# Optimization experiments

Measured on AMD Instinct MI355X. Metric: run time of the kernel, lower is better.

The kernel has to match this reference:

```python
import jax, jax.numpy as jnp
import numpy as np

B, C, H, W = 8, 128, 64, 64
NWIN, HEADS, QKDIM, KVPW, TOPK = 8, 8, 128, 4, 16
SCALE = QKDIM ** -0.5

def _ln(x, g, b, eps):
    mu = x.mean(-1, keepdims=True)
    var = ((x - mu) ** 2).mean(-1, keepdims=True)
    return (x - mu) * jax.lax.rsqrt(var + eps) * g + b

def _conv(x, w, b, pad, groups=1):
    y = jax.lax.conv_general_dilated(x, w, (1, 1), [(pad, pad), (pad, pad)],
        dimension_numbers=('NCHW', 'OIHW', 'NCHW'), feature_group_count=groups)
    return y + b[None, :, None, None]

def setup_inputs():
    key = jax.random.key(0)
    ks = jax.random.split(key, 8)
    s = 0.05
    return {
        't1': jax.random.normal(ks[0], (B, C, H, W), jnp.float32),
        't2': jax.random.normal(ks[1], (B, C, H, W), jnp.float32),
        'pos_w': jax.random.normal(ks[2], (C, 1, 3, 3), jnp.float32) * s,
        'pos_b': jnp.zeros((C,), jnp.float32),
        'cat_w': jax.random.normal(ks[3], (C, 2 * C, 3, 3), jnp.float32) * s,
        'cat_b': jnp.zeros((C,), jnp.float32),
        'ln_cat_g': jnp.ones((C,), jnp.float32),
        'ln_cat_b': jnp.zeros((C,), jnp.float32),
        'ln1_g': jnp.ones((C,), jnp.float32),
        'ln1_b': jnp.zeros((C,), jnp.float32),
        'qkv_w': jax.random.normal(ks[4], (2 * QKDIM + C, C), jnp.float32) * s,
        'qkv_b': jnp.zeros((2 * QKDIM + C,), jnp.float32),
        'lepe_w': jax.random.normal(ks[5], (C, 1, 5, 5), jnp.float32) * s,
        'lepe_b': jnp.zeros((C,), jnp.float32),
        'wo_w': jax.random.normal(ks[6], (C, C), jnp.float32) * s,
        'wo_b': jnp.zeros((C,), jnp.float32),
    }

def _bra_cross(q_in, kv_in, qkv_w, qkv_b, lepe_w, lepe_b, wo_w, wo_b):
    # Bi-level routing cross attention: queries from q_in, keys/values from kv_in (NHWC).
    p = NWIN; wh, ww = H // p, W // p; p2 = p * p
    q = (q_in @ qkv_w.T + qkv_b)[..., :QKDIM]          # (B,H,W,QKDIM)
    kv = (kv_in @ qkv_w.T + qkv_b)[..., QKDIM:]        # (B,H,W,QKDIM+C)

    def win(x):
        c = x.shape[-1]
        return x.reshape(B, p, wh, p, ww, c).transpose(0, 1, 3, 2, 4, 5).reshape(B, p2, wh, ww, c)

    qw, kvw = win(q), win(kv)
    q_pix = qw.reshape(B, p2, wh * ww, QKDIM)
    # adaptive avg-pool each window's kv to KVPW x KVPW ('ada_avgpool')
    f = wh // KVPW
    kv_pix = kvw.reshape(B, p2, KVPW, f, KVPW, f, QKDIM + C).mean(axis=(3, 5))
    kv_pix = kv_pix.reshape(B, p2, KVPW * KVPW, QKDIM + C)
    q_win = qw.mean(axis=(2, 3))                        # (B,p2,QKDIM)
    k_win = kvw[..., :QKDIM].mean(axis=(2, 3))
    # LePE: depthwise 5x5 conv on full-resolution v
    v_full = kv[..., QKDIM:].transpose(0, 3, 1, 2)
    lepe = _conv(v_full, lepe_w, lepe_b, 2, groups=C).transpose(0, 2, 3, 1)
    # region-level routing (detached: diff_routing=False)
    logits = jnp.einsum('bpc,bqc->bpq',
                        jax.lax.stop_gradient(q_win) * SCALE,
                        jax.lax.stop_gradient(k_win))
    _, r_idx = jax.lax.top_k(logits, TOPK)              # (B,p2,TOPK)
    # gather kv of routed regions: (B,p2,TOPK,KVPW^2,QKDIM+C)
    kv_sel = jax.vmap(lambda kvp, idx: kvp[idx])(kv_pix, r_idx)
    k_sel = kv_sel[..., :QKDIM].reshape(B, p2, TOPK * KVPW * KVPW, HEADS, QKDIM // HEADS)
    v_sel = kv_sel[..., QKDIM:].reshape(B, p2, TOPK * KVPW * KVPW, HEADS, C // HEADS)
    q_h = q_pix.reshape(B, p2, wh * ww, HEADS, QKDIM // HEADS)
    attn = jnp.einsum('bpqmc,bpkmc->bpmqk', q_h * SCALE, k_sel)
    attn = jax.nn.softmax(attn, axis=-1)
    out = jnp.einsum('bpmqk,bpkmc->bpqmc', attn, v_sel).reshape(B, p2, wh, ww, C)
    out = out.reshape(B, p, p, wh, ww, C).transpose(0, 1, 3, 2, 4, 5).reshape(B, H, W, C)
    out = out + lepe
    return out @ wo_w.T + wo_b

def reference(t1, t2, pos_w, pos_b, cat_w, cat_b, ln_cat_g, ln_cat_b,
              ln1_g, ln1_b, qkv_w, qkv_b, lepe_w, lepe_b, wo_w, wo_b):
    # Block.forward: depthwise conv positional embedding
    t1 = t1 + _conv(t1, pos_w, pos_b, 1, groups=C)
    t2 = t2 + _conv(t2, pos_w, pos_b, 1, groups=C)
    t1n = t1.transpose(0, 2, 3, 1)
    t2n = t2.transpose(0, 2, 3, 1)
    # RGBConcatConv: cat on channel-last, 3x3 conv, relu(LayerNorm)
    xc = jnp.concatenate([t1n, t2n], axis=3).transpose(0, 3, 1, 2)
    xc = _conv(xc, cat_w, cat_b, 1).transpose(0, 2, 3, 1)
    x = jax.nn.relu(_ln(xc, ln_cat_g, ln_cat_b, 1e-5))
    attn = _bra_cross(_ln(t1n, ln1_g, ln1_b, 1e-6), _ln(t2n, ln1_g, ln1_b, 1e-6),
                      qkv_w, qkv_b, lepe_w, lepe_b, wo_w, wo_b)
    x = x + attn
    return x.transpose(0, 3, 1, 2)
```

## Files before the change

### kernel.cpp

```cpp
#include <hip/hip_runtime.h>
#include <math.h>

typedef unsigned short ushort_t;
typedef __attribute__((ext_vector_type(4))) float f32x4;
typedef __attribute__((ext_vector_type(16))) float f32x16;
typedef __attribute__((ext_vector_type(8))) short bf16x8;

constexpr int B = 8, C = 128, H = 64, W = 64;
constexpr int HEADS = 8, TOPK = 16;
constexpr int P2 = 64;
constexpr float SCALE = 0.0883883476483184405f;

constexpr size_t NPIX    = (size_t)B * H * W;
constexpr size_t OFF_T1C = 0;
constexpr size_t OFF_T2C = OFF_T1C + NPIX * 128;
constexpr size_t OFF_X   = OFF_T2C + NPIX * 128;
constexpr size_t OFF_QB  = OFF_X   + NPIX * 128;
constexpr size_t OFF_KV  = OFF_QB  + NPIX * 64;
constexpr size_t OFF_KVP = OFF_KV  + NPIX * 256;
constexpr size_t OFF_RW1 = OFF_KVP + 524288;
constexpr size_t OFF_RW2 = OFF_RW1 + 524288;
constexpr size_t OFF_KVPT= OFF_KVP + (size_t)B * P2 * 16 * 256;
constexpr size_t OFF_QW  = OFF_KVPT+ (size_t)B * P2 * 128 * 16 / 2;
constexpr size_t OFF_KW  = OFF_QW  + (size_t)B * P2 * 128;
constexpr size_t OFF_RIDX= OFF_KW  + (size_t)B * P2 * 128;
constexpr size_t OFF_WCB = OFF_RIDX+ (size_t)B * P2 * TOPK;
constexpr size_t OFF_QKVB= OFF_WCB + (size_t)9 * 256 * 128;
constexpr size_t OFF_WOB = OFF_QKVB+ (size_t)384 * 128 / 2;
constexpr size_t OFF_T1B = OFF_WOB + 8192;
constexpr size_t OFF_T2B = OFF_T1B + NPIX * 64;

__device__ inline ushort_t f2bf(float f) {
    unsigned u = __float_as_uint(f);
    unsigned r = u + 0x7FFFu + ((u >> 16) & 1u);
    return (ushort_t)(r >> 16);
}
__device__ inline float bf2f(ushort_t u) {
    return __uint_as_float((unsigned)u << 16);
}

__global__ void transpose_weights(const float* __restrict__ qkv_w,
                                  const float* __restrict__ wo_w,
                                  const float* __restrict__ cat_w,
                                  ushort_t* __restrict__ qkvB,
                                  ushort_t* __restrict__ woB,
                                  ushort_t* __restrict__ wcat2) {
    int idx = blockIdx.x * 256 + threadIdx.x;
    if (idx < 384 * 128) qkvB[idx] = f2bf(qkv_w[idx]);
    if (idx < 128 * 128) woB[idx]  = f2bf(wo_w[idx]);
    if (idx < 36 * 8 * 128 * 8) {
        int i  = idx & 7;
        int n  = (idx >> 3) & 127;
        int r  = idx >> 10;
        int lg = r & 3;
        int kk = (r >> 2) & 1;
        int sdd = r >> 3;
        int dd = sdd % 9, q = sdd / 9;
        int ci = q * 64 + kk * 32 + lg * 8 + i;
        wcat2[idx] = f2bf(cat_w[((size_t)n * 256 + ci) * 9 + dd]);
    }
}

__global__ __launch_bounds__(256) void pos_conv_k(
        const float* __restrict__ t1, const float* __restrict__ t2,
        const float* __restrict__ w, const float* __restrict__ bias,
        float* __restrict__ out1, float* __restrict__ out2,
        ushort_t* __restrict__ ob1, ushort_t* __restrict__ ob2) {
    __shared__ float tile[4][32][33];
    int z = blockIdx.z;
    int which = z >> 7, rem = z & 127;
    int b = rem >> 4, y0 = (rem & 15) * 4;
    const float* in = which ? t2 : t1;
    float* outNHWC = which ? out2 : out1;
    ushort_t* outB = which ? ob2 : ob1;
    int c0 = blockIdx.y * 32, x0 = blockIdx.x * 32;
    int tx = threadIdx.x & 31, tg = threadIdx.x >> 5;
    int x = x0 + tx;
    for (int i = 0; i < 4; i++) {
        int cl = tg * 4 + i, c = c0 + cl;
        const float* base = in + (size_t)(b * C + c) * H * W;
        float wv[9];
#pragma unroll
        for (int j = 0; j < 9; j++) wv[j] = w[c * 9 + j];
        float rows[6][3];
#pragma unroll
        for (int yy = 0; yy < 6; yy++) {
            int gy = y0 - 1 + yy;
            bool yok = (gy >= 0 && gy < H);
#pragma unroll
            for (int dx = 0; dx < 3; dx++) {
                int gx = x + dx - 1;
                rows[yy][dx] = (yok && gx >= 0 && gx < W) ? base[gy * W + gx] : 0.f;
            }
        }
        float bb = bias[c];
#pragma unroll
        for (int k = 0; k < 4; k++) {
            float acc = rows[k + 1][1] + bb;
#pragma unroll
            for (int dy = 0; dy < 3; dy++)
#pragma unroll
                for (int dx = 0; dx < 3; dx++)
                    acc += rows[k + dy][dx] * wv[dy * 3 + dx];
            tile[k][cl][tx] = acc;
        }
    }
    __syncthreads();
    for (int k = 0; k < 4; k++)
        for (int i = 0; i < 4; i++) {
            int xl = tg * 4 + i;
            float val = tile[k][tx][xl];
            size_t idx = ((size_t)(b * H + y0 + k) * W + x0 + xl) * 128 + c0 + tx;
            outNHWC[idx] = val;
            outB[idx] = f2bf(val);
        }
}

__global__ __launch_bounds__(512) void catconv_mfma_k(
        const ushort_t* __restrict__ t1b, const ushort_t* __restrict__ t2b,
        const ushort_t* __restrict__ wcat2,
        const float* __restrict__ cat_b,
        const float* __restrict__ g, const float* __restrict__ beta,
        ushort_t* __restrict__ xbuf) {
    __shared__ __align__(16) unsigned char smem[64 * 132 * 4 + 2 * 64 * 4];
    int t = threadIdx.x;
    int lane = t & 63, wv = t >> 6;
    int mw = wv >> 2, nw = wv & 3;
    int l15 = lane & 15, lg = lane >> 4;
    int b = blockIdx.z, y0 = blockIdx.y * 8, x0 = blockIdx.x * 8;

    f32x4 acc[2][2];
#pragma unroll
    for (int m = 0; m < 2; m++)
#pragma unroll
        for (int cf = 0; cf < 2; cf++)
            acc[m][cf] = (f32x4){0.f, 0.f, 0.f, 0.f};

    int pyA[2], pxA[2];
#pragma unroll
    for (int m = 0; m < 2; m++) {
        int p = mw * 32 + m * 16 + l15;
        pyA[m] = p >> 3; pxA[m] = p & 7;
    }

    for (int q = 0; q < 4; q++) {
        __syncthreads();
        {
            const ushort_t* src = (q < 2 ? t1b : t2b);
            int coff = (q & 1) * 64;
            for (int e = t; e < 800; e += 512) {
                int pix = e >> 3, c8 = e & 7;
                int hy = pix / 10, hx = pix - hy * 10;
                int gy = y0 - 1 + hy, gx = x0 - 1 + hx;
                uint4 v = make_uint4(0u, 0u, 0u, 0u);
                if (gy >= 0 && gy < H && gx >= 0 && gx < W)
                    v = *reinterpret_cast<const uint4*>(
                        src + ((size_t)(b * H + gy) * W + gx) * 128 + coff + c8 * 8);
                *reinterpret_cast<uint4*>(smem + pix * 144 + c8 * 16) = v;
            }
        }
        __syncthreads();
#pragma unroll
// ... 1 lines not shown
            int dy = dd / 3, dx = dd - dy * 3;
            const ushort_t* wb = wcat2 + ((size_t)((q * 9 + dd) * 8 + lg) * 128) * 8;
            bf16x8 bfr[2][2];
#pragma unroll
            for (int kk = 0; kk < 2; kk++)
#pragma unroll
                for (int cf = 0; cf < 2; cf++)
                    bfr[kk][cf] = *reinterpret_cast<const bf16x8*>(
                        wb + (size_t)kk * 4096 + (nw * 32 + cf * 16 + l15) * 8);
            bf16x8 af[2][2];
#pragma unroll
            for (int m = 0; m < 2; m++)
#pragma unroll
                for (int kk = 0; kk < 2; kk++)
                    af[m][kk] = *reinterpret_cast<const bf16x8*>(
                        smem + ((pyA[m] + dy) * 10 + pxA[m] + dx) * 144 + kk * 64 + lg * 16);
#pragma unroll
            for (int m = 0; m < 2; m++)
#pragma unroll
                for (int cf = 0; cf < 2; cf++)
#pragma unroll
                    for (int kk = 0; kk < 2; kk++)
                        acc[m][cf] = __builtin_amdgcn_mfma_f32_16x16x32_bf16(
                            af[m][kk], bfr[kk][cf], acc[m][cf], 0, 0, 0);
        }
    }

    __syncthreads();
    float* res = (float*)smem;
    float* mstat = (float*)(smem + 64 * 132 * 4);
#pragma unroll
    for (int cf = 0; cf < 2; cf++) {
        int n = nw * 32 + cf * 16 + l15;
        float cb = cat_b[n];
#pragma unroll
        for (int m = 0; m < 2; m++)
#pragma unroll
            for (int i = 0; i < 4; i++)
                res[(mw * 32 + m * 16 + lg * 4 + i) * 132 + n] = acc[m][cf][i] + cb;
    }
    __syncthreads();
    {
        int pix = t >> 3, sub = t & 7;
        float s1 = 0.f;
#pragma unroll
        for (int j = 0; j < 16; j++) s1 += res[pix * 132 + sub + j * 8];
        s1 += __shfl_xor(s1, 1, 64);
        s1 += __shfl_xor(s1, 2, 64);
        s1 += __shfl_xor(s1, 4, 64);
        float mean = s1 * (1.f / 128.f);
        float s2 = 0.f;
#pragma unroll
        for (int j = 0; j < 16; j++) {
            float d = res[pix * 132 + sub + j * 8] - mean;
            s2 += d * d;
        }
        s2 += __shfl_xor(s2, 1, 64);
        s2 += __shfl_xor(s2, 2, 64);
        s2 += __shfl_xor(s2, 4, 64);
        float inv = rsqrtf(s2 * (1.f / 128.f) + 1e-5f);
        if (sub == 0) { mstat[pix] = mean; mstat[64 + pix] = inv; }
    }
    __syncthreads();
    {
        int c = t & 127, pg = t >> 7;
        float gg = g[c], bb = beta[c];
        for (int j = 0; j < 16; j++) {
            int p2 = j * 4 + pg;
            float v = (res[p2 * 132 + c] - mstat[p2]) * mstat[64 + p2] * gg + bb;
            int py = p2 >> 3, px = p2 & 7;
            xbuf[((size_t)(b * H + y0 + py) * W + x0 + px) * 128 + c] = f2bf(fmaxf(v, 0.f));
        }
    }
}

__global__ __launch_bounds__(256) void ln_qkv_both_k(
        const float* __restrict__ t1c, const float* __restrict__ t2c,
        const float* __restrict__ g, const float* __restrict__ beta,
        const ushort_t* __restrict__ wB,
        const float* __restrict__ bias,
        ushort_t* __restrict__ outQ,
        ushort_t* __restrict__ outKV,
        float* __restrict__ rw1, float* __restrict__ rw2) {
    __shared__ __align__(16) unsigned char ash[64 * 272];
    int t = threadIdx.x;
    int lane = t & 63, wv = t >> 6;
    int which = blockIdx.y;
    const float* in = which ? t2c : t1c;
    float* rw = which ? rw2 : rw1;
    size_t p0 = (size_t)blockIdx.x * 64;
    int bb_ = blockIdx.x >> 6, yy_ = blockIdx.x & 63;
    {
        int row = t >> 2, sub = t & 3;
        const float* src = in + (p0 + row) * 128 + sub * 32;
        float4 v[8];
        float s = 0.f;
#pragma unroll
        for (int j = 0; j < 8; j++) {
            v[j] = *reinterpret_cast<const float4*>(src + j * 4);
            s += v[j].x + v[j].y + v[j].z + v[j].w;
        }
        s += __shfl_xor(s, 1, 64); s += __shfl_xor(s, 2, 64);
        float mean = s * (1.f / 128.f);
        float s2 = 0.f;
#pragma unroll
        for (int j = 0; j < 8; j++) {
            float dx = v[j].x - mean, dy = v[j].y - mean;
            float dz = v[j].z - mean, dw = v[j].w - mean;
            s2 += dx * dx + dy * dy + dz * dz + dw * dw;
        }
        s2 += __shfl_xor(s2, 1, 64); s2 += __shfl_xor(s2, 2, 64);
        float inv = rsqrtf(s2 * (1.f / 128.f) + 1e-6f);
        int wj = wv * 2 + (lane >> 5);
        bool writer = (lane & 28) == 0;
        float* rwp = rw + (((size_t)(bb_ * 8 + wj) * 64 + yy_) * 128) + sub * 32;
#pragma unroll
        for (int j = 0; j < 8; j++) {
            int c = sub * 32 + j * 4;
            float4 gv = *reinterpret_cast<const float4*>(g + c);
            float4 bv = *reinterpret_cast<const float4*>(beta + c);
            float o0 = (v[j].x - mean) * inv * gv.x + bv.x;
            float o1 = (v[j].y - mean) * inv * gv.y + bv.y;
            float o2 = (v[j].z - mean) * inv * gv.z + bv.z;
            float o3 = (v[j].w - mean) * inv * gv.w + bv.w;
            uint2 pk;
            pk.x = (unsigned)f2bf(o0) | ((unsigned)f2bf(o1) << 16);
            pk.y = (unsigned)f2bf(o2) | ((unsigned)f2bf(o3) << 16);
            *reinterpret_cast<uint2*>(ash + row * 272 + c * 2) = pk;
            float r0 = o0, r1 = o1, r2 = o2, r3 = o3;
#pragma unroll
            for (int m = 4; m <= 16; m <<= 1) {
                r0 += __shfl_xor(r0, m, 64);
                r1 += __shfl_xor(r1, m, 64);
                r2 += __shfl_xor(r2, m, 64);
                r3 += __shfl_xor(r3, m, 64);
            }
            if (writer)
                *reinterpret_cast<float4*>(rwp + j * 4) = make_float4(r0, r1, r2, r3);
        }
    }
    __syncthreads();
    int l15 = lane & 15, lg = lane >> 4;
    if (which == 0) {
        f32x4 acc[4][2];
#pragma unroll
        for (int mt = 0; mt < 4; mt++)
#pragma unroll
            for (int nn = 0; nn < 2; nn++)
                acc[mt][nn] = (f32x4){0.f, 0.f, 0.f, 0.f};
#pragma unroll
        for (int ks = 0; ks < 4; ks++) {
            bf16x8 af[4];
#pragma unroll
            for (int mt = 0; mt < 4; mt++)
                af[mt] = *reinterpret_cast<const bf16x8*>(
                    ash + (mt * 16 + l15) * 272 + ks * 64 + lg * 16);
#pragma unroll
            for (int nn = 0; nn < 2; nn++) {
                int n = (wv * 2 + nn) * 16 + l15;
                bf16x8 bfr = *reinterpret_cast<const bf16x8*>(
                    wB + (size_t)n * 128 + ks * 32 + lg * 8);
#pragma unroll
                for (int mt = 0; mt < 4; mt++)
                    acc[mt][nn] = __builtin_amdgcn_mfma_f32_16x16x32_bf16(
                        af[mt], bfr, acc[mt][nn], 0, 0, 0);
            }
        }
#pragma unroll
        for (int nn = 0; nn < 2; nn++) {
            int cg = (wv * 2 + nn) * 16 + l15;
            float bv = bias[cg];
#pragma unroll
            for (int mt = 0; mt < 4; mt++)
#pragma unroll
                for (int i = 0; i < 4; i++) {
                    size_t pix = p0 + mt * 16 + lg * 4 + i;
                    outQ[pix * 128 + cg] = f2bf((acc[mt][nn][i] + bv) * SCALE);
                }
        }
    } else {
        f32x4 acc[4][4];
#pragma unroll
        for (int mt = 0; mt < 4; mt++)
#pragma unroll
            for (int nn = 0; nn < 4; nn++)
                acc[mt][nn] = (f32x4){0.f, 0.f, 0.f, 0.f};
#pragma unroll
        for (int ks = 0; ks < 4; ks++) {
            bf16x8 af[4];
#pragma unroll
            for (int mt = 0; mt < 4; mt++)
                af[mt] = *reinterpret_cast<const bf16x8*>(
                    ash + (mt * 16 + l15) * 272 + ks * 64 + lg * 16);
#pragma unroll
            for (int nn = 0; nn < 4; nn++) {
                int n = 128 + (wv * 4 + nn) * 16 + l15;
                bf16x8 bfr = *reinterpret_cast<const bf16x8*>(
                    wB + (size_t)n * 128 + ks * 32 + lg * 8);
#pragma unroll
                for (int mt = 0; mt < 4; mt++)
                    acc[mt][nn] = __builtin_amdgcn_mfma_f32_16x16x32_bf16(
                        af[mt], bfr, acc[mt][nn], 0, 0, 0);
            }
        }
#pragma unroll
        for (int nn = 0; nn < 4; nn++) {
            int cg = (wv * 4 + nn) * 16 + l15;
            float bv = bias[128 + cg];
#pragma unroll
            for (int mt = 0; mt < 4; mt++)
#pragma unroll
                for (int i = 0; i < 4; i++) {
                    size_t pix = p0 + mt * 16 + lg * 4 + i;
                    outKV[pix * 256 + cg] = f2bf(acc[mt][nn][i] + bv);
                }
        }
    }
}

__global__ __launch_bounds__(256) void route_gemm_k(
        const float* __restrict__ rw1, const float* __restrict__ rw2,
        const float* __restrict__ qkv_w, const float* __restrict__ qkv_b,
        float* __restrict__ qwin, float* __restrict__ kwin) {
    __shared__ float msh[2][8][128];
    int b = blockIdx.y, wi = blockIdx.x;
    int t = threadIdx.x;
    for (int i = t; i < 8 * 128; i += 256) {
        int r = i >> 7, c = i & 127;
        size_t off = (((size_t)(b * 8 + r) * 64) + wi * 8) * 128 + c;
        float s1 = 0.f, s2 = 0.f;
#pragma unroll
        for (int rr = 0; rr < 8; rr++) {
            s1 += rw1[off + rr * 128];
            s2 += rw2[off + rr * 128];
        }
        msh[0][r][c] = s1 * (1.f / 64.f);
        msh[1][r][c] = s2 * (1.f / 64.f);
    }
    __syncthreads();
    int c = t;
    int which = c >> 7;
    const float* wrow = qkv_w + (size_t)c * 128;
    float acc[8];
#pragma unroll
    for (int r = 0; r < 8; r++) acc[r] = 0.f;
    for (int k = 0; k < 128; k++) {
        float wv_ = wrow[k];
#pragma unroll
        for (int r = 0; r < 8; r++) acc[r] += msh[which][r][k] * wv_;
    }
    float bv = qkv_b[c];
#pragma unroll
    for (int r = 0; r < 8; r++) {
        size_t o = ((size_t)b * 64 + wi * 8 + r) * 128 + (c & 127);
        (which ? kwin : qwin)[o] = acc[r] + bv;
    }
}

__global__ __launch_bounds__(64) void route_k(const float* __restrict__ q_win,
                                              const float* __restrict__ k_win,
                                              int* __restrict__ r_idx) {
    int b = blockIdx.y, p = blockIdx.x, j = threadIdx.x;
    const float* qp = q_win + (size_t)(b * 64 + p) * 128;
    const float* kp = k_win + (size_t)(b * 64 + j) * 128;
    float lg = 0.f;
    for (int c = 0; c < 128; c++) lg += qp[c] * kp[c];
    lg *= SCALE;
    for (int it = 0; it < TOPK; it++) {
        float v = lg; int idx = j;
#pragma unroll
        for (int m = 32; m > 0; m >>= 1) {
            float ov = __shfl_xor(v, m, 64);
            int   oi = __shfl_xor(idx, m, 64);
            if (ov > v || (ov == v && oi < idx)) { v = ov; idx = oi; }
        }
        if (j == 0) r_idx[(size_t)(b * 64 + p) * TOPK + it] = idx;
        if (j == idx) lg = -__builtin_inff();
    }
}

__global__ __launch_bounds__(256) void pool_v_k(const ushort_t* __restrict__ kv,
                                                ushort_t* __restrict__ kb,
                                                ushort_t* __restrict__ kvpT,
                                                ushort_t* __restrict__ vpl) {
    int b = blockIdx.y, wdw = blockIdx.x;
    int wi = wdw >> 3, wj = wdw & 7;
    int t = threadIdx.x;
    if (t < 128) {
        float vals[16];
        for (int ry = 0; ry < 4; ry++)
            for (int rx = 0; rx < 4; rx++) {
                float s = 0.f;
                for (int fy = 0; fy < 2; fy++)
                    for (int fx = 0; fx < 2; fx++) {
                        int y = wi * 8 + ry * 2 + fy, x = wj * 8 + rx * 2 + fx;
                        s += bf2f(kv[((size_t)(b * H + y) * W + x) * 256 + t]);
                    }
                vals[ry * 4 + rx] = s * 0.25f;
            }
#pragma unroll
        for (int pos = 0; pos < 16; pos++)
            kb[(((size_t)(b * 64 + wdw)) * 16 + pos) * 128 + t] = f2bf(vals[pos]);
    } else {
        int c = t - 128;
        float ps[4][4];
#pragma unroll
        for (int i = 0; i < 4; i++)
#pragma unroll
            for (int j = 0; j < 4; j++) ps[i][j] = 0.f;
        for (int y = 0; y < 8; y++) {
            union { ushort_t u16[8]; uint4 u4; } raw;
#pragma unroll
            for (int x = 0; x < 8; x++) {
                raw.u16[x] = kv[((size_t)(b * H + wi * 8 + y) * W + wj * 8 + x) * 256 + 128 + c];
                ps[y >> 1][x >> 1] += bf2f(raw.u16[x]);
            }
            *reinterpret_cast<uint4*>(
                vpl + ((size_t)(b * C + c) * H + wi * 8 + y) * W + wj * 8) = raw.u4;
        }
        union { ushort_t u16[16]; uint4 u4[2]; } pk;
#pragma unroll
        for (int ry = 0; ry < 4; ry++)
#pragma unroll
            for (int rx = 0; rx < 4; rx++)
                pk.u16[ry * 4 + rx] = f2bf(ps[ry][rx] * 0.25f);
        size_t base = (((size_t)(b * 64 + wdw)) * 128 + c) * 16;
        *reinterpret_cast<uint4*>(kvpT + base) = pk.u4[0];
        *reinterpret_cast<uint4*>(kvpT + base + 8) = pk.u4[1];
    }
}

__global__ __launch_bounds__(256) void attn_mfma_k(
        const ushort_t* __restrict__ qb,
        const ushort_t* __restrict__ kb,
        const ushort_t* __restrict__ kvpT,
        const int* __restrict__ r_idx,
        ushort_t* __restrict__ o) {
    __shared__ int ridx_sh[16];
    __shared__ float denom_sh[4][32];
    __shared__ __align__(16) ushort_t osh[64][32];

    int b = blockIdx.z, p = blockIdx.x, pair = blockIdx.y;
    int wi = p >> 3, wj = p & 7;
    int t = threadIdx.x;
    int lane = t & 63, wv = t >> 6;
    int l31 = lane & 31, hi = lane >> 5;

    if (t < 16) ridx_sh[t] = r_idx[(size_t)(b * 64 + p) * TOPK + t];
    __syncthreads();

    int hh = wv >> 1, qt = wv & 1;
    int h = pair * 2 + hh;

    int q = qt * 32 + l31;
    int qy = wi * 8 + (q >> 3), qx = wj * 8 + (q & 7);
    bf16x8 qf = *reinterpret_cast<const bf16x8*>(
        qb + ((size_t)(b * H + qy) * W + qx) * 128 + h * 16 + hi * 8);

    const ushort_t* kb_b = kb + (size_t)b * 64 * 16 * 128 + h * 16 + hi * 8;
    const ushort_t* vt_b = kvpT + (size_t)b * 64 * 128 * 16 + (h * 16 + (l31 & 15)) * 16 + hi * 8;

    float m_run = -INFINITY, l_run = 0.f;
// ... 39 lines not shown
                    (__float_as_uint(p_[2 * j + 1]) & 0xFFFF0000u);
#pragma unroll
        for (int j = 0; j < 8; j++) pw_[j] = __shfl_xor(w_[j], 32, 64);
        union { unsigned u[4]; bf16x8 v; } fa0, fa1;
        fa0.u[0] = hi ? pw_[2] : w_[0];
        fa0.u[1] = hi ? pw_[3] : w_[1];
        fa0.u[2] = hi ? w_[2]  : pw_[0];
        fa0.u[3] = hi ? w_[3]  : pw_[1];
        fa1.u[0] = hi ? pw_[6] : w_[4];
        fa1.u[1] = hi ? pw_[7] : w_[5];
        fa1.u[2] = hi ? w_[6]  : pw_[4];
        fa1.u[3] = hi ? w_[7]  : pw_[5];
        opv = __builtin_amdgcn_mfma_f32_32x32x16_bf16(fa0.v, v0, opv, 0, 0, 0);
        opv = __builtin_amdgcn_mfma_f32_32x32x16_bf16(fa1.v, v1, opv, 0, 0, 0);
        kf = kfn; v0 = v0n; v1 = v1n;
    }
    denom_sh[wv][l31] = l_run;
    if (l31 < 16) {
#pragma unroll
        for (int r = 0; r < 16; r++) {
            int qr = (r & 3) + 8 * (r >> 2) + 4 * hi;
            float invd = 1.f / denom_sh[wv][qr];
            osh[qt * 32 + qr][hh * 16 + l31] = f2bf(opv[r] * invd);
        }
    }
    __syncthreads();
    {
        int p_ = t >> 2, seg = t & 3;
        int y = wi * 8 + (p_ >> 3), x = wj * 8 + (p_ & 7);
        *reinterpret_cast<uint4*>(
            o + ((size_t)(b * H + y) * W + x) * 128 + pair * 32 + seg * 8) =
            *reinterpret_cast<const uint4*>(&osh[p_][seg * 8]);
    }
}

__global__ __launch_bounds__(256) void lepe_plane_k(const ushort_t* __restrict__ vpl,
                                                    const float* __restrict__ w,
                                                    const float* __restrict__ bias,
                                                    ushort_t* __restrict__ lep) {
    __shared__ float tile[68][69];
    int c = blockIdx.x, b = blockIdx.y;
    int t = threadIdx.x;
    const ushort_t* plane = vpl + (size_t)(b * C + c) * 4096;
    for (int e = t; e < 68 * 68; e += 256) {
        int row = e / 68, col = e - row * 68;
        int gy = row - 2, gx = col - 2;
        tile[row][col] = (gy >= 0 && gy < 64 && gx >= 0 && gx < 64)
                         ? bf2f(plane[gy * 64 + gx]) : 0.f;
    }
    float wv[25];
#pragma unroll
    for (int j = 0; j < 25; j++) wv[j] = w[c * 25 + j];
    float bb = bias[c];
    __syncthreads();
    int y = t >> 2, x0 = (t & 3) * 16;
    float acc[16];
#pragma unroll
    for (int i = 0; i < 16; i++) acc[i] = bb;
#pragma unroll
    for (int dy = 0; dy < 5; dy++) {
        float vals[20];
#pragma unroll
        for (int j = 0; j < 20; j++) vals[j] = tile[y + dy][x0 + j];
#pragma unroll
        for (int dx = 0; dx < 5; dx++)
#pragma unroll
            for (int i = 0; i < 16; i++)
                acc[i] += vals[i + dx] * wv[dy * 5 + dx];
    }
    ushort_t* dst = lep + (size_t)(b * C + c) * 4096 + y * 64 + x0;
    union { ushort_t u16[16]; uint4 u4[2]; } pk;
#pragma unroll
    for (int i = 0; i < 16; i++) pk.u16[i] = f2bf(acc[i]);
    *reinterpret_cast<uint4*>(dst) = pk.u4[0];
    *reinterpret_cast<uint4*>(dst + 8) = pk.u4[1];
}

__global__ __launch_bounds__(256) void epilogue_mfma_k(
        const ushort_t* __restrict__ o,
        const ushort_t* __restrict__ lep,
        const ushort_t* __restrict__ xbuf,
        const ushort_t* __restrict__ woB,
        const float* __restrict__ wo_b,
        float* __restrict__ out) {
    __shared__ __align__(16) unsigned char smem[128 * 68 * 4];
    ushort_t* ash = (ushort_t*)smem;
    float* res = (float*)smem;
    int t = threadIdx.x, lane = t & 63, wv = t >> 6;
    int bid = blockIdx.x;
    int b = bid >> 6, y = bid & 63;
    size_t p0 = (size_t)bid * 64;

#pragma unroll
    for (int k = 0; k < 4; k++) {
        int e = k * 256 + t;
        int c = e >> 3, xg = e & 7;
        union { uint4 u4; ushort_t u16[8]; } v;
        v.u4 = *reinterpret_cast<const uint4*>(
            lep + (((size_t)(b * C + c) * 64 + y) * 64) + xg * 8);
#pragma unroll
        for (int j = 0; j < 8; j++) ash[(xg * 8 + j) * 136 + c] = v.u16[j];
    }
    __syncthreads();
    {
        int x = t >> 2, sub = t & 3;
        const ushort_t* op = o + (p0 + x) * 128 + sub * 32;
        ushort_t* ap = ash + x * 136 + sub * 32;
#pragma unroll
// ... 71 lines not shown
    const float* ln_cat_b= (const float*)d_in[7];
    const float* ln1_g   = (const float*)d_in[8];
    const float* ln1_b   = (const float*)d_in[9];
    const float* qkv_w   = (const float*)d_in[10];
    const float* qkv_b   = (const float*)d_in[11];
    const float* lepe_w  = (const float*)d_in[12];
    const float* lepe_b  = (const float*)d_in[13];
    const float* wo_w    = (const float*)d_in[14];
    const float* wo_b    = (const float*)d_in[15];

    float* ws    = (float*)d_ws;
    float* t1c   = ws + OFF_T1C;
    float* t2c   = ws + OFF_T2C;
    ushort_t* xbuf = (ushort_t*)(ws + OFF_X);
    ushort_t* qbuf = (ushort_t*)(ws + OFF_QB);
    ushort_t* kvbuf= (ushort_t*)(ws + OFF_KV);
    ushort_t* kb   = (ushort_t*)(ws + OFF_KVP);
    float* rw1   = ws + OFF_RW1;
    float* rw2   = ws + OFF_RW2;
    ushort_t* kvpT = (ushort_t*)(ws + OFF_KVPT);
    float* qwin  = ws + OFF_QW;
    float* kwin  = ws + OFF_KW;
    int*   ridx  = (int*)(ws + OFF_RIDX);
    ushort_t* wcat2 = (ushort_t*)(ws + OFF_WCB);
    ushort_t* qkvB  = (ushort_t*)(ws + OFF_QKVB);
    ushort_t* woB   = (ushort_t*)(ws + OFF_WOB);
    ushort_t* t1b   = (ushort_t*)(ws + OFF_T1B);
    ushort_t* t2b   = (ushort_t*)(ws + OFF_T2B);
    ushort_t* obuf  = (ushort_t*)(ws + OFF_T1C);
    ushort_t* vpl   = (ushort_t*)(ws + OFF_T2C);
    ushort_t* lep   = (ushort_t*)(ws + OFF_KV);
    float* out   = (float*)d_out;

    transpose_weights<<<dim3((36 * 8 * 128 * 8 + 255) / 256), 256, 0, stream>>>(
        qkv_w, wo_w, cat_w, qkvB, woB, wcat2);
    pos_conv_k<<<dim3(2, 4, 256), 256, 0, stream>>>(
        t1, t2, pos_w, pos_b, t1c, t2c, t1b, t2b);
    catconv_mfma_k<<<dim3(8, 8, 8), 512, 0, stream>>>(
        t1b, t2b, wcat2, cat_b, ln_cat_g, ln_cat_b, xbuf);
    ln_qkv_both_k<<<dim3(512, 2), 256, 0, stream>>>(
        t1c, t2c, ln1_g, ln1_b, qkvB, qkv_b, qbuf, kvbuf, rw1, rw2);
    route_gemm_k<<<dim3(8, B), 256, 0, stream>>>(rw1, rw2, qkv_w, qkv_b, qwin, kwin);
    route_k<<<dim3(64, B), 64, 0, stream>>>(qwin, kwin, ridx);
    pool_v_k<<<dim3(64, B), 256, 0, stream>>>(kvbuf, kb, kvpT, vpl);
    attn_mfma_k<<<dim3(64, 4, B), 256, 0, stream>>>(qbuf, kb, kvpT, ridx, obuf);
    lepe_plane_k<<<dim3(C, B), 256, 0, stream>>>(vpl, lepe_w, lepe_b, lep);
    epilogue_mfma_k<<<dim3(512), 256, 0, stream>>>(obuf, lep, xbuf, woB, wo_b, out);
}
```

Baseline: 167.9 us.

## Merge independent kernels into horizontally fused launches to cut launch count

Combines independent stages into shared launches by splitting the grid on block index: weight conversion with the positional conv, the cat-conv with the LN+QKV projection, the routing GEMM with V pooling, and routing top-k with the LePE conv. This drops the launch count from ten to six and lets independent work fill the GPU together. The LN+QKV branch now runs in 512-thread blocks covering 128 pixels. The cost is heterogeneous blocks that share the larger shared-memory and register footprint, which may lower occupancy.

```diff
diff --git a/kernel.cpp b/kernel.cpp
--- a/kernel.cpp
+++ b/kernel.cpp
@@ -39,49 +39,51 @@
     return __uint_as_float((unsigned)u << 16);
 }
 
-__global__ void transpose_weights(const float* __restrict__ qkv_w,
-                                  const float* __restrict__ wo_w,
-                                  const float* __restrict__ cat_w,
-                                  ushort_t* __restrict__ qkvB,
-                                  ushort_t* __restrict__ woB,
-                                  ushort_t* __restrict__ wcat2) {
-    int idx = blockIdx.x * 256 + threadIdx.x;
-    if (idx < 384 * 128) qkvB[idx] = f2bf(qkv_w[idx]);
-    if (idx < 128 * 128) woB[idx]  = f2bf(wo_w[idx]);
-    if (idx < 36 * 8 * 128 * 8) {
-        int i  = idx & 7;
-        int n  = (idx >> 3) & 127;
-        int r  = idx >> 10;
-        int lg = r & 3;
-        int kk = (r >> 2) & 1;
-        int sdd = r >> 3;
-        int dd = sdd % 9, q = sdd / 9;
-        int ci = q * 64 + kk * 32 + lg * 8 + i;
-        wcat2[idx] = f2bf(cat_w[((size_t)n * 256 + ci) * 9 + dd]);
-    }
-}
-
-__global__ __launch_bounds__(256) void pos_conv_k(
+__global__ __launch_bounds__(256) void prep_pos_k(
         const float* __restrict__ t1, const float* __restrict__ t2,
-        const float* __restrict__ w, const float* __restrict__ bias,
+        const float* __restrict__ pos_w, const float* __restrict__ pos_b,
+        const float* __restrict__ qkv_w, const float* __restrict__ wo_w,
+        const float* __restrict__ cat_w,
+        ushort_t* __restrict__ qkvB, ushort_t* __restrict__ woB,
+        ushort_t* __restrict__ wcat2,
         float* __restrict__ out1, float* __restrict__ out2,
         ushort_t* __restrict__ ob1, ushort_t* __restrict__ ob2) {
     __shared__ float tile[4][32][33];
-    int z = blockIdx.z;
+    int bid = blockIdx.x;
+    int t = threadIdx.x;
+    if (bid < 1152) {
+        int idx = bid * 256 + t;
+        if (idx < 384 * 128) qkvB[idx] = f2bf(qkv_w[idx]);
+        if (idx < 128 * 128) woB[idx]  = f2bf(wo_w[idx]);
+        if (idx < 36 * 8 * 128 * 8) {
+            int i  = idx & 7;
+            int n  = (idx >> 3) & 127;
+            int r  = idx >> 10;
+            int lg = r & 3;
+            int kk = (r >> 2) & 1;
+            int sdd = r >> 3;
+            int dd = sdd % 9, q = sdd / 9;
+            int ci = q * 64 + kk * 32 + lg * 8 + i;
+            wcat2[idx] = f2bf(cat_w[((size_t)n * 256 + ci) * 9 + dd]);
+        }
+        return;
+    }
+    int pb = bid - 1152;
+    int xb = pb & 1, cg = (pb >> 1) & 3, z = pb >> 3;
     int which = z >> 7, rem = z & 127;
     int b = rem >> 4, y0 = (rem & 15) * 4;
     const float* in = which ? t2 : t1;
     float* outNHWC = which ? out2 : out1;
     ushort_t* outB = which ? ob2 : ob1;
-    int c0 = blockIdx.y * 32, x0 = blockIdx.x * 32;
-    int tx = threadIdx.x & 31, tg = threadIdx.x >> 5;
+    int c0 = cg * 32, x0 = xb * 32;
+    int tx = t & 31, tg = t >> 5;
     int x = x0 + tx;
     for (int i = 0; i < 4; i++) {
         int cl = tg * 4 + i, c = c0 + cl;
         const float* base = in + (size_t)(b * C + c) * H * W;
         float wv[9];
 #pragma unroll
-        for (int j = 0; j < 9; j++) wv[j] = w[c * 9 + j];
+        for (int j = 0; j < 9; j++) wv[j] = pos_w[c * 9 + j];
         float rows[6][3];
 #pragma unroll
         for (int yy = 0; yy < 6; yy++) {
@@ -93,7 +95,7 @@
                 rows[yy][dx] = (yok && gx >= 0 && gx < W) ? base[gy * W + gx] : 0.f;
             }
         }
-        float bb = bias[c];
+        float bb = pos_b[c];
 #pragma unroll
         for (int k = 0; k < 4; k++) {
             float acc = rows[k + 1][1] + bb;
@@ -116,18 +118,164 @@
         }
 }
 
-__global__ __launch_bounds__(512) void catconv_mfma_k(
+__global__ __launch_bounds__(512) void cat_ln_k(
         const ushort_t* __restrict__ t1b, const ushort_t* __restrict__ t2b,
         const ushort_t* __restrict__ wcat2,
         const float* __restrict__ cat_b,
-        const float* __restrict__ g, const float* __restrict__ beta,
-        ushort_t* __restrict__ xbuf) {
-    __shared__ __align__(16) unsigned char smem[64 * 132 * 4 + 2 * 64 * 4];
+        const float* __restrict__ gcat, const float* __restrict__ bcat,
+        ushort_t* __restrict__ xbuf,
+        const float* __restrict__ t1c, const float* __restrict__ t2c,
+        const float* __restrict__ g1, const float* __restrict__ b1,
+        const ushort_t* __restrict__ qkvB, const float* __restrict__ qkv_b,
+        ushort_t* __restrict__ outQ, ushort_t* __restrict__ outKV,
+        float* __restrict__ rw1, float* __restrict__ rw2) {
+    __shared__ __align__(16) unsigned char smem[64 * 272 * 2];
+    int bid = blockIdx.x;
     int t = threadIdx.x;
     int lane = t & 63, wv = t >> 6;
+    int l15 = lane & 15, lg = lane >> 4;
+
+    if (bid < 512) {
+        unsigned char* ash = smem;
+        int which = bid >> 8;
+        int blk = bid & 255;
+        const float* in = which ? t2c : t1c;
+        float* rw = which ? rw2 : rw1;
+        size_t p0 = (size_t)blk * 128;
+        int bb_ = blk >> 5, y0 = (blk & 31) * 2;
+        {
+            int row = t >> 2, sub = t & 3;
+            const float* src = in + (p0 + row) * 128 + sub * 32;
+            float4 v[8];
+            float s = 0.f;
+#pragma unroll
+            for (int j = 0; j < 8; j++) {
+                v[j] = *reinterpret_cast<const float4*>(src + j * 4);
+                s += v[j].x + v[j].y + v[j].z + v[j].w;
+            }
+            s += __shfl_xor(s, 1, 64); s += __shfl_xor(s, 2, 64);
+            float mean = s * (1.f / 128.f);
+            float s2 = 0.f;
+#pragma unroll
+            for (int j = 0; j < 8; j++) {
+                float dx = v[j].x - mean, dy = v[j].y - mean;
+                float dz = v[j].z - mean, dw = v[j].w - mean;
+                s2 += dx * dx + dy * dy + dz * dz + dw * dw;
+            }
+            s2 += __shfl_xor(s2, 1, 64); s2 += __shfl_xor(s2, 2, 64);
+            float inv = rsqrtf(s2 * (1.f / 128.f) + 1e-6f);
+            int wj = (wv & 3) * 2 + (lane >> 5);
+            int yy_ = y0 + (wv >> 2);
+            bool writer = (lane & 28) == 0;
+            float* rwp = rw + (((size_t)(bb_ * 8 + wj) * 64 + yy_) * 128) + sub * 32;
+#pragma unroll
+            for (int j = 0; j < 8; j++) {
+                int c = sub * 32 + j * 4;
+                float4 gv = *reinterpret_cast<const float4*>(g1 + c);
+                float4 bv = *reinterpret_cast<const float4*>(b1 + c);
+                float o0 = (v[j].x - mean) * inv * gv.x + bv.x;
+                float o1 = (v[j].y - mean) * inv * gv.y + bv.y;
+                float o2 = (v[j].z - mean) * inv * gv.z + bv.z;
+                float o3 = (v[j].w - mean) * inv * gv.w + bv.w;
+                uint2 pk;
+                pk.x = (unsigned)f2bf(o0) | ((unsigned)f2bf(o1) << 16);
+                pk.y = (unsigned)f2bf(o2) | ((unsigned)f2bf(o3) << 16);
+                *reinterpret_cast<uint2*>(ash + row * 272 + c * 2) = pk;
+                float r0 = o0, r1 = o1, r2 = o2, r3 = o3;
+#pragma unroll
+                for (int m = 4; m <= 16; m <<= 1) {
+                    r0 += __shfl_xor(r0, m, 64);
+                    r1 += __shfl_xor(r1, m, 64);
+                    r2 += __shfl_xor(r2, m, 64);
+                    r3 += __shfl_xor(r3, m, 64);
+                }
+                if (writer)
+                    *reinterpret_cast<float4*>(rwp + j * 4) = make_float4(r0, r1, r2, r3);
+            }
+        }
+        __syncthreads();
+        int mh = wv >> 2, nw = wv & 3;
+        if (which == 0) {
+            f32x4 acc[4][2];
+#pragma unroll
+            for (int mt = 0; mt < 4; mt++)
+#pragma unroll
+                for (int nn = 0; nn < 2; nn++)
+                    acc[mt][nn] = (f32x4){0.f, 0.f, 0.f, 0.f};
+#pragma unroll
+            for (int ks = 0; ks < 4; ks++) {
+                bf16x8 af[4];
+#pragma unroll
+                for (int mt = 0; mt < 4; mt++)
+                    af[mt] = *reinterpret_cast<const bf16x8*>(
+                        ash + (mh * 64 + mt * 16 + l15) * 272 + ks * 64 + lg * 16);
+#pragma unroll
+                for (int nn = 0; nn < 2; nn++) {
+                    int n = (nw * 2 + nn) * 16 + l15;
+                    bf16x8 bfr = *reinterpret_cast<const bf16x8*>(
+                        qkvB + (size_t)n * 128 + ks * 32 + lg * 8);
+#pragma unroll
+                    for (int mt = 0; mt < 4; mt++)
+                        acc[mt][nn] = __builtin_amdgcn_mfma_f32_16x16x32_bf16(
+                            af[mt], bfr, acc[mt][nn], 0, 0, 0);
+                }
+            }
+#pragma unroll
+            for (int nn = 0; nn < 2; nn++) {
+                int cg = (nw * 2 + nn) * 16 + l15;
+                float bv = qkv_b[cg];
+#pragma unroll
+                for (int mt = 0; mt < 4; mt++)
+#pragma unroll
+                    for (int i = 0; i < 4; i++) {
+                        size_t pix = p0 + mh * 64 + mt * 16 + lg * 4 + i;
+                        outQ[pix * 128 + cg] = f2bf((acc[mt][nn][i] + bv) * SCALE);
+                    }
+            }
+        } else {
+            f32x4 acc[4][4];
+#pragma unroll
+            for (int mt = 0; mt < 4; mt++)
+#pragma unroll
+                for (int nn = 0; nn < 4; nn++)
+                    acc[mt][nn] = (f32x4){0.f, 0.f, 0.f, 0.f};
+#pragma unroll
+            for (int ks = 0; ks < 4; ks++) {
+                bf16x8 af[4];
+#pragma unroll
+                for (int mt = 0; mt < 4; mt++)
+                    af[mt] = *reinterpret_cast<const bf16x8*>(
+                        ash + (mh * 64 + mt * 16 + l15) * 272 + ks * 64 + lg * 16);
+#pragma unroll
+                for (int nn = 0; nn < 4; nn++) {
+                    int n = 128 + (nw * 4 + nn) * 16 + l15;
+                    bf16x8 bfr = *reinterpret_cast<const bf16x8*>(
+                        qkvB + (size_t)n * 128 + ks * 32 + lg * 8);
+#pragma unroll
+                    for (int mt = 0; mt < 4; mt++)
+                        acc[mt][nn] = __builtin_amdgcn_mfma_f32_16x16x32_bf16(
+                            af[mt], bfr, acc[mt][nn], 0, 0, 0);
+                }
+            }
+#pragma unroll
+            for (int nn = 0; nn < 4; nn++) {
+                int cg = (nw * 4 + nn) * 16 + l15;
+                float bv = qkv_b[128 + cg];
+#pragma unroll
+                for (int mt = 0; mt < 4; mt++)
+#pragma unroll
+                    for (int i = 0; i < 4; i++) {
+                        size_t pix = p0 + mh * 64 + mt * 16 + lg * 4 + i;
+                        outKV[pix * 256 + cg] = f2bf(acc[mt][nn][i] + bv);
+                    }
+            }
+        }
+        return;
+    }
+
+    int cb = bid - 512;
     int mw = wv >> 2, nw = wv & 3;
-    int l15 = lane & 15, lg = lane >> 4;
-    int b = blockIdx.z, y0 = blockIdx.y * 8, x0 = blockIdx.x * 8;
+    int b = cb >> 6, y0 = ((cb >> 3) & 7) * 8, x0 = (cb & 7) * 8;
 
     f32x4 acc[2][2];
 #pragma unroll
@@ -195,12 +343,12 @@
 #pragma unroll
     for (int cf = 0; cf < 2; cf++) {
         int n = nw * 32 + cf * 16 + l15;
-        float cb = cat_b[n];
+        float cbv = cat_b[n];
 #pragma unroll
         for (int m = 0; m < 2; m++)
 #pragma unroll
             for (int i = 0; i < 4; i++)
-                res[(mw * 32 + m * 16 + lg * 4 + i) * 132 + n] = acc[m][cf][i] + cb;
+                res[(mw * 32 + m * 16 + lg * 4 + i) * 132 + n] = acc[m][cf][i] + cbv;
     }
     __syncthreads();
     {
@@ -227,7 +375,7 @@
     __syncthreads();
     {
         int c = t & 127, pg = t >> 7;
-        float gg = g[c], bb = beta[c];
+        float gg = gcat[c], bb = bcat[c];
         for (int j = 0; j < 16; j++) {
             int p2 = j * 4 + pg;
             float v = (res[p2 * 132 + c] - mstat[p2]) * mstat[64 + p2] * gg + bb;
@@ -237,218 +385,53 @@
     }
 }
 
-__global__ __launch_bounds__(256) void ln_qkv_both_k(
-        const float* __restrict__ t1c, const float* __restrict__ t2c,
-        const float* __restrict__ g, const float* __restrict__ beta,
-        const ushort_t* __restrict__ wB,
-        const float* __restrict__ bias,
-        ushort_t* __restrict__ outQ,
-        ushort_t* __restrict__ outKV,
-        float* __restrict__ rw1, float* __restrict__ rw2) {
-    __shared__ __align__(16) unsigned char ash[64 * 272];
-    int t = threadIdx.x;
-    int lane = t & 63, wv = t >> 6;
-    int which = blockIdx.y;
-    const float* in = which ? t2c : t1c;
-    float* rw = which ? rw2 : rw1;
-    size_t p0 = (size_t)blockIdx.x * 64;
-    int bb_ = blockIdx.x >> 6, yy_ = blockIdx.x & 63;
-    {
-        int row = t >> 2, sub = t & 3;
-        const float* src = in + (p0 + row) * 128 + sub * 32;
-        float4 v[8];
-        float s = 0.f;
-#pragma unroll
-        for (int j = 0; j < 8; j++) {
-            v[j] = *reinterpret_cast<const float4*>(src + j * 4);
-            s += v[j].x + v[j].y + v[j].z + v[j].w;
-        }
-        s += __shfl_xor(s, 1, 64); s += __shfl_xor(s, 2, 64);
-        float mean = s * (1.f / 128.f);
-        float s2 = 0.f;
-#pragma unroll
-        for (int j = 0; j < 8; j++) {
-            float dx = v[j].x - mean, dy = v[j].y - mean;
-            float dz = v[j].z - mean, dw = v[j].w - mean;
-            s2 += dx * dx + dy * dy + dz * dz + dw * dw;
-        }
-        s2 += __shfl_xor(s2, 1, 64); s2 += __shfl_xor(s2, 2, 64);
-        float inv = rsqrtf(s2 * (1.f / 128.f) + 1e-6f);
-        int wj = wv * 2 + (lane >> 5);
-        bool writer = (lane & 28) == 0;
-        float* rwp = rw + (((size_t)(bb_ * 8 + wj) * 64 + yy_) * 128) + sub * 32;
-#pragma unroll
-        for (int j = 0; j < 8; j++) {
-            int c = sub * 32 + j * 4;
-            float4 gv = *reinterpret_cast<const float4*>(g + c);
-            float4 bv = *reinterpret_cast<const float4*>(beta + c);
-            float o0 = (v[j].x - mean) * inv * gv.x + bv.x;
-            float o1 = (v[j].y - mean) * inv * gv.y + bv.y;
-            float o2 = (v[j].z - mean) * inv * gv.z + bv.z;
-            float o3 = (v[j].w - mean) * inv * gv.w + bv.w;
-            uint2 pk;
-            pk.x = (unsigned)f2bf(o0) | ((unsigned)f2bf(o1) << 16);
-            pk.y = (unsigned)f2bf(o2) | ((unsigned)f2bf(o3) << 16);
-            *reinterpret_cast<uint2*>(ash + row * 272 + c * 2) = pk;
-            float r0 = o0, r1 = o1, r2 = o2, r3 = o3;
-#pragma unroll
-            for (int m = 4; m <= 16; m <<= 1) {
-                r0 += __shfl_xor(r0, m, 64);
-                r1 += __shfl_xor(r1, m, 64);
-                r2 += __shfl_xor(r2, m, 64);
-                r3 += __shfl_xor(r3, m, 64);
-            }
-            if (writer)
-                *reinterpret_cast<float4*>(rwp + j * 4) = make_float4(r0, r1, r2, r3);
-        }
-    }
-    __syncthreads();
-    int l15 = lane & 15, lg = lane >> 4;
-    if (which == 0) {
-        f32x4 acc[4][2];
-#pragma unroll
-        for (int mt = 0; mt < 4; mt++)
-#pragma unroll
-            for (int nn = 0; nn < 2; nn++)
-                acc[mt][nn] = (f32x4){0.f, 0.f, 0.f, 0.f};
-#pragma unroll
-        for (int ks = 0; ks < 4; ks++) {
-            bf16x8 af[4];
-#pragma unroll
-            for (int mt = 0; mt < 4; mt++)
-                af[mt] = *reinterpret_cast<const bf16x8*>(
-                    ash + (mt * 16 + l15) * 272 + ks * 64 + lg * 16);
-#pragma unroll
-            for (int nn = 0; nn < 2; nn++) {
-                int n = (wv * 2 + nn) * 16 + l15;
-                bf16x8 bfr = *reinterpret_cast<const bf16x8*>(
-                    wB + (size_t)n * 128 + ks * 32 + lg * 8);
-#pragma unroll
-                for (int mt = 0; mt < 4; mt++)
-                    acc[mt][nn] = __builtin_amdgcn_mfma_f32_16x16x32_bf16(
-                        af[mt], bfr, acc[mt][nn], 0, 0, 0);
-            }
-        }
-#pragma unroll
-        for (int nn = 0; nn < 2; nn++) {
-            int cg = (wv * 2 + nn) * 16 + l15;
-            float bv = bias[cg];
-#pragma unroll
-            for (int mt = 0; mt < 4; mt++)
-#pragma unroll
-                for (int i = 0; i < 4; i++) {
-                    size_t pix = p0 + mt * 16 + lg * 4 + i;
-                    outQ[pix * 128 + cg] = f2bf((acc[mt][nn][i] + bv) * SCALE);
-                }
-        }
-    } else {
-        f32x4 acc[4][4];
-#pragma unroll
-        for (int mt = 0; mt < 4; mt++)
-#pragma unroll
-            for (int nn = 0; nn < 4; nn++)
-                acc[mt][nn] = (f32x4){0.f, 0.f, 0.f, 0.f};
-#pragma unroll
-        for (int ks = 0; ks < 4; ks++) {
-            bf16x8 af[4];
-#pragma unroll
-            for (int mt = 0; mt < 4; mt++)
-                af[mt] = *reinterpret_cast<const bf16x8*>(
-                    ash + (mt * 16 + l15) * 272 + ks * 64 + lg * 16);
-#pragma unroll
-            for (int nn = 0; nn < 4; nn++) {
-                int n = 128 + (wv * 4 + nn) * 16 + l15;
-                bf16x8 bfr = *reinterpret_cast<const bf16x8*>(
-                    wB + (size_t)n * 128 + ks * 32 + lg * 8);
-#pragma unroll
-                for (int mt = 0; mt < 4; mt++)
-                    acc[mt][nn] = __builtin_amdgcn_mfma_f32_16x16x32_bf16(
-                        af[mt], bfr, acc[mt][nn], 0, 0, 0);
-            }
-        }
-#pragma unroll
-        for (int nn = 0; nn < 4; nn++) {
-            int cg = (wv * 4 + nn) * 16 + l15;
-            float bv = bias[128 + cg];
-#pragma unroll
-            for (int mt = 0; mt < 4; mt++)
-#pragma unroll
-                for (int i = 0; i < 4; i++) {
-                    size_t pix = p0 + mt * 16 + lg * 4 + i;
-                    outKV[pix * 256 + cg] = f2bf(acc[mt][nn][i] + bv);
-                }
-        }
-    }
-}
-
-__global__ __launch_bounds__(256) void route_gemm_k(
+__global__ __launch_bounds__(256) void route_pool_k(
         const float* __restrict__ rw1, const float* __restrict__ rw2,
         const float* __restrict__ qkv_w, const float* __restrict__ qkv_b,
-        float* __restrict__ qwin, float* __restrict__ kwin) {
+        float* __restrict__ qwin, float* __restrict__ kwin,
+        const ushort_t* __restrict__ kv,
+        ushort_t* __restrict__ kb, ushort_t* __restrict__ kvpT,
+        ushort_t* __restrict__ vpl) {
     __shared__ float msh[2][8][128];
-    int b = blockIdx.y, wi = blockIdx.x;
+    int bid = blockIdx.x;
     int t = threadIdx.x;
-    for (int i = t; i < 8 * 128; i += 256) {
-        int r = i >> 7, c = i & 127;
-        size_t off = (((size_t)(b * 8 + r) * 64) + wi * 8) * 128 + c;
-        float s1 = 0.f, s2 = 0.f;
-#pragma unroll
-        for (int rr = 0; rr < 8; rr++) {
-            s1 += rw1[off + rr * 128];
-            s2 += rw2[off + rr * 128];
-        }
-        msh[0][r][c] = s1 * (1.f / 64.f);
-        msh[1][r][c] = s2 * (1.f / 64.f);
-    }
-    __syncthreads();
-    int c = t;
-    int which = c >> 7;
-    const float* wrow = qkv_w + (size_t)c * 128;
-    float acc[8];
-#pragma unroll
-    for (int r = 0; r < 8; r++) acc[r] = 0.f;
-    for (int k = 0; k < 128; k++) {
-        float wv_ = wrow[k];
-#pragma unroll
-        for (int r = 0; r < 8; r++) acc[r] += msh[which][r][k] * wv_;
-    }
-    float bv = qkv_b[c];
-#pragma unroll
-    for (int r = 0; r < 8; r++) {
-        size_t o = ((size_t)b * 64 + wi * 8 + r) * 128 + (c & 127);
-        (which ? kwin : qwin)[o] = acc[r] + bv;
-    }
-}
-
-__global__ __launch_bounds__(64) void route_k(const float* __restrict__ q_win,
-                                              const float* __restrict__ k_win,
-                                              int* __restrict__ r_idx) {
-    int b = blockIdx.y, p = blockIdx.x, j = threadIdx.x;
-    const float* qp = q_win + (size_t)(b * 64 + p) * 128;
-    const float* kp = k_win + (size_t)(b * 64 + j) * 128;
-    float lg = 0.f;
-    for (int c = 0; c < 128; c++) lg += qp[c] * kp[c];
-    lg *= SCALE;
-    for (int it = 0; it < TOPK; it++) {
-        float v = lg; int idx = j;
-#pragma unroll
-        for (int m = 32; m > 0; m >>= 1) {
-            float ov = __shfl_xor(v, m, 64);
-            int   oi = __shfl_xor(idx, m, 64);
-            if (ov > v || (ov == v && oi < idx)) { v = ov; idx = oi; }
-        }
-        if (j == 0) r_idx[(size_t)(b * 64 + p) * TOPK + it] = idx;
-        if (j == idx) lg = -__builtin_inff();
-    }
-}
-
-__global__ __launch_bounds__(256) void pool_v_k(const ushort_t* __restrict__ kv,
-                                                ushort_t* __restrict__ kb,
-                                                ushort_t* __restrict__ kvpT,
-                                                ushort_t* __restrict__ vpl) {
-    int b = blockIdx.y, wdw = blockIdx.x;
+    if (bid < 64) {
+        int b = bid >> 3, wi = bid & 7;
+        for (int i = t; i < 8 * 128; i += 256) {
+            int r = i >> 7, c = i & 127;
+            size_t off = (((size_t)(b * 8 + r) * 64) + wi * 8) * 128 + c;
+            float s1 = 0.f, s2 = 0.f;
+#pragma unroll
+            for (int rr = 0; rr < 8; rr++) {
+                s1 += rw1[off + rr * 128];
+                s2 += rw2[off + rr * 128];
+            }
+            msh[0][r][c] = s1 * (1.f / 64.f);
+            msh[1][r][c] = s2 * (1.f / 64.f);
+        }
+        __syncthreads();
+        int c = t;
+        int which = c >> 7;
+        const float* wrow = qkv_w + (size_t)c * 128;
+        float acc[8];
+#pragma unroll
+        for (int r = 0; r < 8; r++) acc[r] = 0.f;
+        for (int k = 0; k < 128; k++) {
+            float wv_ = wrow[k];
+#pragma unroll
+            for (int r = 0; r < 8; r++) acc[r] += msh[which][r][k] * wv_;
+        }
+        float bv = qkv_b[c];
+#pragma unroll
+        for (int r = 0; r < 8; r++) {
+            size_t o = ((size_t)b * 64 + wi * 8 + r) * 128 + (c & 127);
+            (which ? kwin : qwin)[o] = acc[r] + bv;
+        }
+        return;
+    }
+    int pb = bid - 64;
+    int b = pb >> 6, wdw = pb & 63;
     int wi = wdw >> 3, wj = wdw & 7;
-    int t = threadIdx.x;
     if (t < 128) {
         float vals[16];
         for (int ry = 0; ry < 4; ry++)
@@ -491,6 +474,73 @@
         *reinterpret_cast<uint4*>(kvpT + base) = pk.u4[0];
         *reinterpret_cast<uint4*>(kvpT + base + 8) = pk.u4[1];
     }
+}
+
+__global__ __launch_bounds__(256) void route_lepe_k(
+        const float* __restrict__ q_win, const float* __restrict__ k_win,
+        int* __restrict__ r_idx,
+        const ushort_t* __restrict__ vpl,
+        const float* __restrict__ w, const float* __restrict__ bias,
+        ushort_t* __restrict__ lep) {
+    __shared__ float tile[68][69];
+    int bid = blockIdx.x;
+    int t = threadIdx.x;
+    if (bid < 128) {
+        int b = bid >> 4, p = (bid & 15) * 4 + (t >> 6);
+        int j = t & 63;
+        const float* qp = q_win + (size_t)(b * 64 + p) * 128;
+        const float* kp = k_win + (size_t)(b * 64 + j) * 128;
+        float lg = 0.f;
+        for (int c = 0; c < 128; c++) lg += qp[c] * kp[c];
+        lg *= SCALE;
+        for (int it = 0; it < TOPK; it++) {
+            float v = lg; int idx = j;
+#pragma unroll
+            for (int m = 32; m > 0; m >>= 1) {
+                float ov = __shfl_xor(v, m, 64);
+                int   oi = __shfl_xor(idx, m, 64);
+                if (ov > v || (ov == v && oi < idx)) { v = ov; idx = oi; }
+            }
+            if (j == 0) r_idx[(size_t)(b * 64 + p) * TOPK + it] = idx;
+            if (j == idx) lg = -__builtin_inff();
+        }
+        return;
+    }
+    int lb = bid - 128;
+    int c = lb & 127, b = lb >> 7;
+    const ushort_t* plane = vpl + (size_t)(b * C + c) * 4096;
+    for (int e = t; e < 68 * 68; e += 256) {
+        int row = e / 68, col = e - row * 68;
+        int gy = row - 2, gx = col - 2;
+        tile[row][col] = (gy >= 0 && gy < 64 && gx >= 0 && gx < 64)
+                         ? bf2f(plane[gy * 64 + gx]) : 0.f;
+    }
+    float wv[25];
+#pragma unroll
+    for (int j = 0; j < 25; j++) wv[j] = w[c * 25 + j];
+    float bb = bias[c];
+    __syncthreads();
+    int y = t >> 2, x0 = (t & 3) * 16;
+    float acc[16];
+#pragma unroll
+    for (int i = 0; i < 16; i++) acc[i] = bb;
+#pragma unroll
+    for (int dy = 0; dy < 5; dy++) {
+        float vals[20];
+#pragma unroll
+        for (int j = 0; j < 20; j++) vals[j] = tile[y + dy][x0 + j];
+#pragma unroll
+        for (int dx = 0; dx < 5; dx++)
+#pragma unroll
+            for (int i = 0; i < 16; i++)
+                acc[i] += vals[i + dx] * wv[dy * 5 + dx];
+    }
+    ushort_t* dst = lep + (size_t)(b * C + c) * 4096 + y * 64 + x0;
+    union { ushort_t u16[16]; uint4 u4[2]; } pk;
+#pragma unroll
+    for (int i = 0; i < 16; i++) pk.u16[i] = f2bf(acc[i]);
+    *reinterpret_cast<uint4*>(dst) = pk.u4[0];
+    *reinterpret_cast<uint4*>(dst + 8) = pk.u4[1];
 }
 
 __global__ __launch_bounds__(256) void attn_mfma_k(
@@ -596,48 +646,6 @@
             o + ((size_t)(b * H + y) * W + x) * 128 + pair * 32 + seg * 8) =
             *reinterpret_cast<const uint4*>(&osh[p_][seg * 8]);
     }
-}
-
-__global__ __launch_bounds__(256) void lepe_plane_k(const ushort_t* __restrict__ vpl,
-                                                    const float* __restrict__ w,
-                                                    const float* __restrict__ bias,
-                                                    ushort_t* __restrict__ lep) {
-    __shared__ float tile[68][69];
-    int c = blockIdx.x, b = blockIdx.y;
-    int t = threadIdx.x;
-    const ushort_t* plane = vpl + (size_t)(b * C + c) * 4096;
-    for (int e = t; e < 68 * 68; e += 256) {
-        int row = e / 68, col = e - row * 68;
-        int gy = row - 2, gx = col - 2;
-        tile[row][col] = (gy >= 0 && gy < 64 && gx >= 0 && gx < 64)
-                         ? bf2f(plane[gy * 64 + gx]) : 0.f;
-    }
-    float wv[25];
-#pragma unroll
-    for (int j = 0; j < 25; j++) wv[j] = w[c * 25 + j];
-    float bb = bias[c];
-    __syncthreads();
-    int y = t >> 2, x0 = (t & 3) * 16;
-    float acc[16];
-#pragma unroll
-    for (int i = 0; i < 16; i++) acc[i] = bb;
-#pragma unroll
-    for (int dy = 0; dy < 5; dy++) {
-        float vals[20];
-#pragma unroll
-        for (int j = 0; j < 20; j++) vals[j] = tile[y + dy][x0 + j];
-#pragma unroll
-        for (int dx = 0; dx < 5; dx++)
-#pragma unroll
-            for (int i = 0; i < 16; i++)
-                acc[i] += vals[i + dx] * wv[dy * 5 + dx];
-    }
-    ushort_t* dst = lep + (size_t)(b * C + c) * 4096 + y * 64 + x0;
-    union { ushort_t u16[16]; uint4 u4[2]; } pk;
-#pragma unroll
-    for (int i = 0; i < 16; i++) pk.u16[i] = f2bf(acc[i]);
-    *reinterpret_cast<uint4*>(dst) = pk.u4[0];
-    *reinterpret_cast<uint4*>(dst + 8) = pk.u4[1];
 }
 
 __global__ __launch_bounds__(256) void epilogue_mfma_k(
@@ -775,18 +783,16 @@
     ushort_t* lep   = (ushort_t*)(ws + OFF_KV);
     float* out   = (float*)d_out;
 
-    transpose_weights<<<dim3((36 * 8 * 128 * 8 + 255) / 256), 256, 0, stream>>>(
-        qkv_w, wo_w, cat_w, qkvB, woB, wcat2);
-    pos_conv_k<<<dim3(2, 4, 256), 256, 0, stream>>>(
-        t1, t2, pos_w, pos_b, t1c, t2c, t1b, t2b);
-    catconv_mfma_k<<<dim3(8, 8, 8), 512, 0, stream>>>(
-        t1b, t2b, wcat2, cat_b, ln_cat_g, ln_cat_b, xbuf);
-    ln_qkv_both_k<<<dim3(512, 2), 256, 0, stream>>>(
+    prep_pos_k<<<3200, 256, 0, stream>>>(
+        t1, t2, pos_w, pos_b, qkv_w, wo_w, cat_w,
+        qkvB, woB, wcat2, t1c, t2c, t1b, t2b);
+    cat_ln_k<<<1024, 512, 0, stream>>>(
+        t1b, t2b, wcat2, cat_b, ln_cat_g, ln_cat_b, xbuf,
         t1c, t2c, ln1_g, ln1_b, qkvB, qkv_b, qbuf, kvbuf, rw1, rw2);
-    route_gemm_k<<<dim3(8, B), 256, 0, stream>>>(rw1, rw2, qkv_w, qkv_b, qwin, kwin);
-    route_k<<<dim3(64, B), 64, 0, stream>>>(qwin, kwin, ridx);
-    pool_v_k<<<dim3(64, B), 256, 0, stream>>>(kvbuf, kb, kvpT, vpl);
+    route_pool_k<<<576, 256, 0, stream>>>(
+        rw1, rw2, qkv_w, qkv_b, qwin, kwin, kvbuf, kb, kvpT, vpl);
+    route_lepe_k<<<1152, 256, 0, stream>>>(
+        qwin, kwin, ridx, vpl, lepe_w, lepe_b, lep);
     attn_mfma_k<<<dim3(64, 4, B), 256, 0, stream>>>(qbuf, kb, kvpT, ridx, obuf);
-    lepe_plane_k<<<dim3(C, B), 256, 0, stream>>>(vpl, lepe_w, lepe_b, lep);
-    epilogue_mfma_k<<<dim3(512), 256, 0, stream>>>(obuf, lep, xbuf, woB, wo_b, out);
-}
+    epilogue_mfma_k<<<512, 256, 0, stream>>>(obuf, lep, xbuf, woB, wo_b, out);
+}
```

New measurement: 157.8 us, median of 2. 6.1% less time.
